# Kernel optimization log

Hardware: AMD Instinct MI355X
Metric: run time of the kernel (lower is better)

## Reference

```python
import jax, jax.numpy as jnp
import numpy as np


def setup_inputs() -> dict:
    key = jax.random.key(0)
    k1, k2, k3, k4 = jax.random.split(key, 4)
    B, T, E, H = 8, 2048, 1024, 64
    x = jax.random.normal(k1, (B, T, E), dtype=jnp.float32)
    # scale params like typical init to keep logits sane
    Wk = jax.random.normal(k2, (E, H), dtype=jnp.float32) * (E ** -0.5)
    Wq = jax.random.normal(k3, (E, H), dtype=jnp.float32) * (E ** -0.5)
    Wv = jax.random.normal(k4, (E, H), dtype=jnp.float32) * (E ** -0.5)
    return {"x": x, "Wk": Wk, "Wq": Wq, "Wv": Wv}


def reference(x, Wk, Wq, Wv):
    # x: [B, T, E]; Wk/Wq/Wv: [E, H]
    T = x.shape[1]
    H = Wk.shape[1]
    k = jnp.einsum('bte,eh->bth', x, Wk)
    q = jnp.einsum('bte,eh->bth', x, Wq)
    v = jnp.einsum('bte,eh->bth', x, Wv)
    # scaled scores [B, T, T]
    wei = jnp.einsum('bqh,bkh->bqk', q, k) * (H ** -0.5)
    causal = jnp.tril(jnp.ones((T, T), dtype=bool))  # tril buffer
    wei = jnp.where(causal, wei, -jnp.inf)
    wei = jax.nn.softmax(wei, axis=-1)
    # dropout p=0.0 (eval): identity
    return jnp.einsum('bqk,bkh->bqh', wei, v)
```

## Files before the change

kernel.cpp:

```cpp
#include <hip/hip_runtime.h>
#include <math.h>

constexpr int B_ = 8, T_ = 2048, E_ = 1024, H_ = 64;
constexpr long BT = (long)B_ * T_;

typedef __attribute__((ext_vector_type(8))) short bf16x8;
typedef __attribute__((ext_vector_type(4))) float f32x4;

__device__ inline unsigned short bf16_rne(float f) {
    union { float f; unsigned u; } v; v.f = f;
    unsigned u = v.u + (0x7FFFu + ((v.u >> 16) & 1u));
    return (unsigned short)(u >> 16);
}
__device__ inline unsigned pack_bf16x2(float lo, float hi) {
    unsigned r;
    asm("v_cvt_pk_bf16_f32 %0, %1, %2" : "=v"(r) : "v"(lo), "v"(hi));
    return r;
}

__device__ inline void load_lds16(const void* g, void* l) {
    __builtin_amdgcn_global_load_lds(
        (const __attribute__((address_space(1))) void*)(uintptr_t)g,
        (__attribute__((address_space(3))) void*)(unsigned)(uintptr_t)l,
        16, 0, 0);
}

constexpr float QS = 0.18033688011112042f;

__global__ __launch_bounds__(256) void wt_build_k(
    const float* __restrict__ Wk, const float* __restrict__ Wq,
    const float* __restrict__ Wv, unsigned short* __restrict__ Wt)
{
    const int d    = blockIdx.x * 256 + threadIdx.x;
    const int tile = d >> 6;
    const int lq   = d & 63;
    const int quad = lq >> 4;
    const int l16  = lq & 15;
    const int kc   = tile / 12;
    const int nt   = tile - kc * 12;
    const int n    = nt * 16 + l16;

    const float* src; int col; float s = 1.0f;
    if (n < 64)       { src = Wk; col = n; }
    else if (n < 128) { src = Wq; col = n - 64; s = QS; }
    else              { src = Wv; col = n - 128; }

    const int kk0 = kc * 32 + quad * 8;
    const float* sp = src + (size_t)kk0 * H_ + col;
    unsigned p[4];
    #pragma unroll
    for (int jj = 0; jj < 4; jj++)
        p[jj] = pack_bf16x2(sp[(2 * jj) * H_] * s, sp[(2 * jj + 1) * H_] * s);
    *(uint4*)(Wt + (size_t)d * 8) = make_uint4(p[0], p[1], p[2], p[3]);
}

struct Bfr { bf16x8 b0, b1, b2; };

__global__ __launch_bounds__(512) void qkv_mfma_k(
    const float* __restrict__ x, const unsigned short* __restrict__ Wt,
    unsigned short* __restrict__ kO, unsigned short* __restrict__ qO,
    unsigned short* __restrict__ vfO)
{
    __shared__ float4 xs[3][32][16];
    __shared__ unsigned short VL[32][66];

    const int t    = threadIdx.x;
    const int w    = t >> 6;
    const int l    = t & 63;
    const int l16  = l & 15;
    const int quad = l >> 4;
    const int rg   = w >> 2;
    const int nq   = w & 3;
    const int row0 = blockIdx.x * 32 + rg * 16;
    const int row0b = blockIdx.x * 32;

    const int rr = w * 4 + (l >> 4);
    const int cc = l & 15;
    const int gg = cc ^ (rr & 7);
    const float* gsrc = x + (size_t)(row0b + rr) * E_ + gg * 4;

    const int r  = rg * 16 + l16;
    const int rx = r & 7;

    auto LB = [&](int it, Bfr& F0, Bfr& F1) {
        const unsigned short* p0 = Wt + (size_t)((it * 2) * 12 + nq * 3) * 512 + (size_t)l * 8;
        F0.b0 = *(const bf16x8*)(p0);
        F0.b1 = *(const bf16x8*)(p0 + 512);
        F0.b2 = *(const bf16x8*)(p0 + 1024);
        const unsigned short* p1 = p0 + 12 * 512;
        F1.b0 = *(const bf16x8*)(p1);
        F1.b1 = *(const bf16x8*)(p1 + 512);
        F1.b2 = *(const bf16x8*)(p1 + 1024);
    };
    auto DMA = [&](int it) {
        load_lds16(gsrc + it * 64, &xs[it % 3][rr][cc]);
    };

    f32x4 acc[3];
    #pragma unroll
    for (int n = 0; n < 3; n++) acc[n] = (f32x4){0.f, 0.f, 0.f, 0.f};

    Bfr Bf[2][2];
    DMA(0);
    LB(0, Bf[0][0], Bf[0][1]);
    DMA(1);

    #pragma unroll
    for (int it = 0; it < 16; ++it) {
        if (it == 15) asm volatile("s_waitcnt vmcnt(6)" ::: "memory");
        else          asm volatile("s_waitcnt vmcnt(7)" ::: "memory");
        __builtin_amdgcn_s_barrier();
        __builtin_amdgcn_sched_barrier(0);

        if (it + 1 < 16) LB(it + 1, Bf[(it + 1) & 1][0], Bf[(it + 1) & 1][1]);
        if (it + 2 < 16) DMA(it + 2);

        const int pc = it & 1;
        const int bsel = it % 3;
        #pragma unroll
        for (int kk = 0; kk < 2; ++kk) {
            const int G0 = kk * 8 + quad * 2;
            float4 fa = xs[bsel][r][G0 ^ rx];
            float4 fb = xs[bsel][r][(G0 + 1) ^ rx];

            union { bf16x8 v; unsigned u[4]; } av;
            av.u[0] = pack_bf16x2(fa.x, fa.y);
            av.u[1] = pack_bf16x2(fa.z, fa.w);
            av.u[2] = pack_bf16x2(fb.x, fb.y);
            av.u[3] = pack_bf16x2(fb.z, fb.w);

            Bfr& F = Bf[pc][kk];
            acc[0] = __builtin_amdgcn_mfma_f32_16x16x32_bf16(av.v, F.b0, acc[0], 0, 0, 0);
            acc[1] = __builtin_amdgcn_mfma_f32_16x16x32_bf16(av.v, F.b1, acc[1], 0, 0, 0);
            acc[2] = __builtin_amdgcn_mfma_f32_16x16x32_bf16(av.v, F.b2, acc[2], 0, 0, 0);
        }
    }

    #pragma unroll
    for (int n = 0; n < 3; n++) {
        const int gn = nq * 3 + n;
        const int hb = gn * 16 + l16;
        if (gn < 4) {
            #pragma unroll
            for (int rr2 = 0; rr2 < 4; rr2++) {
                const int row = row0 + quad * 4 + rr2;
                kO[(size_t)row * H_ + hb] = bf16_rne(acc[n][rr2]);
            }
        } else if (gn < 8) {
            #pragma unroll
            for (int rr2 = 0; rr2 < 4; rr2++) {
                const int row = row0 + quad * 4 + rr2;
                qO[(size_t)row * H_ + (hb - 64)] = bf16_rne(acc[n][rr2]);
            }
        } else {
            #pragma unroll
            for (int rr2 = 0; rr2 < 4; rr2++)
                VL[rg * 16 + quad * 4 + rr2][(gn - 8) * 16 + l16] = bf16_rne(acc[n][rr2]);
        }
    }
    __syncthreads();

    if (t < 256) {
        const int g  = t >> 6;
        const int lf = t & 15;
        const int qf = (t >> 4) & 3;
        unsigned pk[4];
        #pragma unroll
        for (int jj = 0; jj < 4; jj++) {
            const int p0 = qf * 8 + 2 * jj;
            const int i0 = (p0 >> 1) | ((p0 & 1) << 4);
            const int p1 = p0 + 1;
            const int i1 = (p1 >> 1) | ((p1 & 1) << 4);
            pk[jj] = (unsigned)VL[i0][g * 16 + lf]
                   | ((unsigned)VL[i1][g * 16 + lf] << 16);
        }
        const int tile = blockIdx.x;
        *(uint4*)(vfO + ((size_t)tile * 4 + g) * 512 + (size_t)(t & 63) * 8) =
            make_uint4(pk[0], pk[1], pk[2], pk[3]);
    }
}

struct Kfr { bf16x8 k00, k01, k10, k11; };
struct Vfr { bf16x8 v0, v1, v2, v3; };

__global__ __launch_bounds__(512) void attn_mfma(
    const unsigned short* __restrict__ q,
    const unsigned short* __restrict__ k,
    const unsigned short* __restrict__ vf,
    float* __restrict__ out)
{
    __shared__ unsigned short Pl[8][2][16 * 40];
    __shared__ float Ot[8][16][68];
    __shared__ float LsW[8][16];

    const int t    = threadIdx.x;
    const int w    = t >> 6;
    const int l    = t & 63;
    const int l16  = l & 15;
    const int quad = l >> 4;

    const int b  = blockIdx.x & 7;
    const int p  = blockIdx.x >> 3;

    const unsigned short* kbp = k  + (size_t)b * T_ * H_ + (size_t)l16 * H_ + quad * 8;
    const unsigned short* vfb = vf + (size_t)b * 64 * 2048 + (size_t)l * 8;
    unsigned short* Pw0 = &Pl[w][0][0];
    unsigned short* Pw1 = &Pl[w][1][0];

    for (int ph = 0; ph < 2; ++ph) {
        const int qt = ph ? (127 - p) : p;
        const int t0 = qt * 16;
        const int nk = t0 / 32 + 1;

        const size_t qoff = ((size_t)b * T_ + t0 + l16) * H_ + quad * 8;
        bf16x8 aq0 = *(const bf16x8*)(q + qoff);
        bf16x8 aq1 = *(const bf16x8*)(q + qoff + 32);

        f32x4 o[4];
        #pragma unroll
        for (int g = 0; g < 4; g++) o[g] = (f32x4){0.f, 0.f, 0.f, 0.f};
        float ls[4] = {0.f, 0.f, 0.f, 0.f};

        auto LK = [&](int kt, Kfr& K) {
            const unsigned short* kp = kbp + (size_t)kt * 32 * H_;
            K.k00 = *(const bf16x8*)(kp);
            K.k01 = *(const bf16x8*)(kp + 32);
            K.k10 = *(const bf16x8*)(kp + 16 * H_);
            K.k11 = *(const bf16x8*)(kp + 16 * H_ + 32);
        };
        auto LV = [&](int kt, Vfr& V) {
            const unsigned short* vp = vfb + (size_t)kt * 2048;
            V.v0 = *(const bf16x8*)(vp);
            V.v1 = *(const bf16x8*)(vp + 512);
            V.v2 = *(const bf16x8*)(vp + 1024);
            V.v3 = *(const bf16x8*)(vp + 1536);
        };
        auto QKSM = [&](int kt, const Kfr& K, unsigned short* Pw) {
            f32x4 s0 = (f32x4){0.f, 0.f, 0.f, 0.f};
            f32x4 s1 = (f32x4){0.f, 0.f, 0.f, 0.f};
            s0 = __builtin_amdgcn_mfma_f32_16x16x32_bf16(aq0, K.k00, s0, 0, 0, 0);
            s0 = __builtin_amdgcn_mfma_f32_16x16x32_bf16(aq1, K.k01, s0, 0, 0, 0);
            s1 = __builtin_amdgcn_mfma_f32_16x16x32_bf16(aq0, K.k10, s1, 0, 0, 0);
            s1 = __builtin_amdgcn_mfma_f32_16x16x32_bf16(aq1, K.k11, s1, 0, 0, 0);
            const int kbase = kt * 32;
            if (kbase + 31 > t0) {
                const int rowb = t0 + quad * 4;
                #pragma unroll
                for (int r = 0; r < 4; r++) {
                    if (kbase + l16 > rowb + r)      s0[r] = -3.0e38f;
                    if (kbase + 16 + l16 > rowb + r) s1[r] = -3.0e38f;
                }
            }
            #pragma unroll
            for (int r = 0; r < 4; r++) {
                float p0 = exp2f(s0[r]);
                float p1 = exp2f(s1[r]);
                ls[r] += p0 + p1;
                *(unsigned*)(Pw + (quad * 4 + r) * 40 + 2 * l16) = pack_bf16x2(p0, p1);
            }
        };
        auto PRD = [&](const unsigned short* Pw) -> bf16x8 {
            return *(const bf16x8*)(Pw + l16 * 40 + quad * 8);
        };
        auto PV = [&](bf16x8 ap, const Vfr& V) {
            o[0] = __builtin_amdgcn_mfma_f32_16x16x32_bf16(ap, V.v0, o[0], 0, 0, 0);
            o[1] = __builtin_amdgcn_mfma_f32_16x16x32_bf16(ap, V.v1, o[1], 0, 0, 0);
            o[2] = __builtin_amdgcn_mfma_f32_16x16x32_bf16(ap, V.v2, o[2], 0, 0, 0);
            o[3] = __builtin_amdgcn_mfma_f32_16x16x32_bf16(ap, V.v3, o[3], 0, 0, 0);
        };

        int kt = w;
        if (kt < nk) {
            Kfr KA, KB; Vfr VA, VB;
            LK(kt, KA);
            if (kt + 8 < nk) LK(kt + 8, KB);
            LV(kt, VA);
            QKSM(kt, KA, Pw0);
            kt += 8;
            if (kt >= nk) {
                bf16x8 ap = PRD(Pw0);
                PV(ap, VA);
            } else {
                for (;;) {
                    if (kt + 8 < nk) LK(kt + 8, KA);
                    LV(kt, VB);
                    __builtin_amdgcn_sched_barrier(0);
                    { bf16x8 ap = PRD(Pw0); QKSM(kt, KB, Pw1); PV(ap, VA); }
                    kt += 8;
                    if (kt >= nk) { bf16x8 ap = PRD(Pw1); PV(ap, VB); break; }
                    if (kt + 8 < nk) LK(kt + 8, KB);
                    LV(kt, VA);
                    __builtin_amdgcn_sched_barrier(0);
                    { bf16x8 ap = PRD(Pw1); QKSM(kt, KA, Pw0); PV(ap, VB); }
                    kt += 8;
                    if (kt >= nk) { bf16x8 ap = PRD(Pw0); PV(ap, VA); break; }
                }
            }
        }

        #pragma unroll
        for (int r = 0; r < 4; r++) {
            float s = ls[r];
            s += __shfl_xor(s, 1);
            s += __shfl_xor(s, 2);
            s += __shfl_xor(s, 4);
            s += __shfl_xor(s, 8);
            ls[r] = s;
        }

        if (l16 == 0) {
            #pragma unroll
            for (int r = 0; r < 4; r++) LsW[w][quad * 4 + r] = ls[r];
        }
        #pragma unroll
        for (int g = 0; g < 4; g++)
            #pragma unroll
            for (int r = 0; r < 4; r++)
                Ot[w][quad * 4 + r][g * 16 + l16] = o[g][r];
        __syncthreads();

        {
            const int col = l;
            #pragma unroll
            for (int rr = 0; rr < 2; ++rr) {
                const int row = w * 2 + rr;
                float L = 0.f, sv = 0.f;
                #pragma unroll
                for (int w2 = 0; w2 < 8; ++w2) {
                    L  += LsW[w2][row];
                    sv += Ot[w2][row][col];
                }
                out[((size_t)b * T_ + t0 + row) * H_ + col] = sv / L;
            }
        }
        __syncthreads();
    }
}

extern "C" void kernel_launch(void* const* d_in, const int* in_sizes, int n_in,
                              void* d_out, int out_size, void* d_ws, size_t ws_size,
                              hipStream_t stream)
{
    const float* x  = (const float*)d_in[0];
    const float* Wk = (const float*)d_in[1];
    const float* Wq = (const float*)d_in[2];
    const float* Wv = (const float*)d_in[3];

    unsigned short* wt    = (unsigned short*)d_ws;
    unsigned short* kbuf  = wt + 24576 * 8;
    unsigned short* qbuf  = kbuf + BT * H_;
    unsigned short* vfbuf = qbuf + BT * H_;
    float* outp = (float*)d_out;

    wt_build_k<<<96, 256, 0, stream>>>(Wk, Wq, Wv, wt);
    qkv_mfma_k<<<(B_ * T_) / 32, 512, 0, stream>>>(x, wt, kbuf, qbuf, vfbuf);
    attn_mfma<<<512, 512, 0, stream>>>(qbuf, kbuf, vfbuf, outp);
}
```

Baseline: 140.4 us.

## Split attention over key chunks into partial blocks plus separate reduction kernel

Replaces the 512-block, 8-wave attention kernel, which paired light and heavy query tiles, with a split-K scheme. Each 256-thread block handles one 16-row query tile and one chunk of up to 8 key tiles, then writes unnormalized partial outputs and row sums to a workspace. A second kernel sums the chunks and normalizes. This aims to improve load balance and occupancy across CUs, at the cost of an extra launch, workspace traffic, many early-exiting empty blocks, and no software pipelining across key tiles within a wave.

```diff
diff --git a/kernel.cpp b/kernel.cpp
--- a/kernel.cpp
+++ b/kernel.cpp
@@ -183,15 +183,15 @@
 struct Kfr { bf16x8 k00, k01, k10, k11; };
 struct Vfr { bf16x8 v0, v1, v2, v3; };
 
-__global__ __launch_bounds__(512) void attn_mfma(
+__global__ __launch_bounds__(256) void attn_part(
     const unsigned short* __restrict__ q,
     const unsigned short* __restrict__ k,
     const unsigned short* __restrict__ vf,
-    float* __restrict__ out)
-{
-    __shared__ unsigned short Pl[8][2][16 * 40];
-    __shared__ float Ot[8][16][68];
-    __shared__ float LsW[8][16];
+    float* __restrict__ part)
+{
+    __shared__ unsigned short Pl[4][2][16 * 40];
+    __shared__ float Ot[4][16][68];
+    __shared__ float LsW[4][16];
 
     const int t    = threadIdx.x;
     const int w    = t >> 6;
@@ -200,141 +200,149 @@
     const int quad = l >> 4;
 
     const int b  = blockIdx.x & 7;
-    const int p  = blockIdx.x >> 3;
+    const int rblk = blockIdx.x >> 3;
+    const int qt = rblk / 9;
+    const int ci = rblk - qt * 9;
+
+    const int nk = qt / 2 + 1;
+    const int c  = (nk + 7) >> 3;
+    if (ci >= c) return;
+
+    const int t0  = qt * 16;
+    const int kt0 = ci * 8;
+    const int nt  = min(8, nk - kt0);
+
+    const size_t qoff = ((size_t)b * T_ + t0 + l16) * H_ + quad * 8;
+    bf16x8 aq0 = *(const bf16x8*)(q + qoff);
+    bf16x8 aq1 = *(const bf16x8*)(q + qoff + 32);
 
     const unsigned short* kbp = k  + (size_t)b * T_ * H_ + (size_t)l16 * H_ + quad * 8;
     const unsigned short* vfb = vf + (size_t)b * 64 * 2048 + (size_t)l * 8;
     unsigned short* Pw0 = &Pl[w][0][0];
     unsigned short* Pw1 = &Pl[w][1][0];
 
-    for (int ph = 0; ph < 2; ++ph) {
-        const int qt = ph ? (127 - p) : p;
-        const int t0 = qt * 16;
-        const int nk = t0 / 32 + 1;
-
-        const size_t qoff = ((size_t)b * T_ + t0 + l16) * H_ + quad * 8;
-        bf16x8 aq0 = *(const bf16x8*)(q + qoff);
-        bf16x8 aq1 = *(const bf16x8*)(q + qoff + 32);
-
-        f32x4 o[4];
-        #pragma unroll
-        for (int g = 0; g < 4; g++) o[g] = (f32x4){0.f, 0.f, 0.f, 0.f};
-        float ls[4] = {0.f, 0.f, 0.f, 0.f};
-
-        auto LK = [&](int kt, Kfr& K) {
-            const unsigned short* kp = kbp + (size_t)kt * 32 * H_;
-            K.k00 = *(const bf16x8*)(kp);
-            K.k01 = *(const bf16x8*)(kp + 32);
-            K.k10 = *(const bf16x8*)(kp + 16 * H_);
-            K.k11 = *(const bf16x8*)(kp + 16 * H_ + 32);
-        };
-        auto LV = [&](int kt, Vfr& V) {
-            const unsigned short* vp = vfb + (size_t)kt * 2048;
-            V.v0 = *(const bf16x8*)(vp);
-            V.v1 = *(const bf16x8*)(vp + 512);
-            V.v2 = *(const bf16x8*)(vp + 1024);
-            V.v3 = *(const bf16x8*)(vp + 1536);
-        };
-        auto QKSM = [&](int kt, const Kfr& K, unsigned short* Pw) {
-            f32x4 s0 = (f32x4){0.f, 0.f, 0.f, 0.f};
-            f32x4 s1 = (f32x4){0.f, 0.f, 0.f, 0.f};
-            s0 = __builtin_amdgcn_mfma_f32_16x16x32_bf16(aq0, K.k00, s0, 0, 0, 0);
-            s0 = __builtin_amdgcn_mfma_f32_16x16x32_bf16(aq1, K.k01, s0, 0, 0, 0);
-            s1 = __builtin_amdgcn_mfma_f32_16x16x32_bf16(aq0, K.k10, s1, 0, 0, 0);
-            s1 = __builtin_amdgcn_mfma_f32_16x16x32_bf16(aq1, K.k11, s1, 0, 0, 0);
-            const int kbase = kt * 32;
-            if (kbase + 31 > t0) {
-                const int rowb = t0 + quad * 4;
-                #pragma unroll
-                for (int r = 0; r < 4; r++) {
-                    if (kbase + l16 > rowb + r)      s0[r] = -3.0e38f;
-                    if (kbase + 16 + l16 > rowb + r) s1[r] = -3.0e38f;
-                }
-            }
+    f32x4 o[4];
+    #pragma unroll
+    for (int g = 0; g < 4; g++) o[g] = (f32x4){0.f, 0.f, 0.f, 0.f};
+    float ls[4] = {0.f, 0.f, 0.f, 0.f};
+
+    auto LK = [&](int kt, Kfr& K) {
+        const unsigned short* kp = kbp + (size_t)kt * 32 * H_;
+        K.k00 = *(const bf16x8*)(kp);
+        K.k01 = *(const bf16x8*)(kp + 32);
+        K.k10 = *(const bf16x8*)(kp + 16 * H_);
+        K.k11 = *(const bf16x8*)(kp + 16 * H_ + 32);
+    };
+    auto LV = [&](int kt, Vfr& V) {
+        const unsigned short* vp = vfb + (size_t)kt * 2048;
+        V.v0 = *(const bf16x8*)(vp);
+        V.v1 = *(const bf16x8*)(vp + 512);
+        V.v2 = *(const bf16x8*)(vp + 1024);
+        V.v3 = *(const bf16x8*)(vp + 1536);
+    };
+    auto QKSM = [&](int kt, const Kfr& K, unsigned short* Pw) {
+        f32x4 s0 = (f32x4){0.f, 0.f, 0.f, 0.f};
+        f32x4 s1 = (f32x4){0.f, 0.f, 0.f, 0.f};
+        s0 = __builtin_amdgcn_mfma_f32_16x16x32_bf16(aq0, K.k00, s0, 0, 0, 0);
+        s0 = __builtin_amdgcn_mfma_f32_16x16x32_bf16(aq1, K.k01, s0, 0, 0, 0);
+        s1 = __builtin_amdgcn_mfma_f32_16x16x32_bf16(aq0, K.k10, s1, 0, 0, 0);
+        s1 = __builtin_amdgcn_mfma_f32_16x16x32_bf16(aq1, K.k11, s1, 0, 0, 0);
+        const int kbase = kt * 32;
+        if (kbase + 31 > t0) {
+            const int rowb = t0 + quad * 4;
             #pragma unroll
             for (int r = 0; r < 4; r++) {
-                float p0 = exp2f(s0[r]);
-                float p1 = exp2f(s1[r]);
-                ls[r] += p0 + p1;
-                *(unsigned*)(Pw + (quad * 4 + r) * 40 + 2 * l16) = pack_bf16x2(p0, p1);
+                if (kbase + l16 > rowb + r)      s0[r] = -3.0e38f;
+                if (kbase + 16 + l16 > rowb + r) s1[r] = -3.0e38f;
             }
-        };
-        auto PRD = [&](const unsigned short* Pw) -> bf16x8 {
-            return *(const bf16x8*)(Pw + l16 * 40 + quad * 8);
-        };
-        auto PV = [&](bf16x8 ap, const Vfr& V) {
-            o[0] = __builtin_amdgcn_mfma_f32_16x16x32_bf16(ap, V.v0, o[0], 0, 0, 0);
-            o[1] = __builtin_amdgcn_mfma_f32_16x16x32_bf16(ap, V.v1, o[1], 0, 0, 0);
-            o[2] = __builtin_amdgcn_mfma_f32_16x16x32_bf16(ap, V.v2, o[2], 0, 0, 0);
-            o[3] = __builtin_amdgcn_mfma_f32_16x16x32_bf16(ap, V.v3, o[3], 0, 0, 0);
-        };
-
-        int kt = w;
-        if (kt < nk) {
-            Kfr KA, KB; Vfr VA, VB;
-            LK(kt, KA);
-            if (kt + 8 < nk) LK(kt + 8, KB);
-            LV(kt, VA);
-            QKSM(kt, KA, Pw0);
-            kt += 8;
-            if (kt >= nk) {
-                bf16x8 ap = PRD(Pw0);
-                PV(ap, VA);
-            } else {
-                for (;;) {
-                    if (kt + 8 < nk) LK(kt + 8, KA);
-                    LV(kt, VB);
-                    __builtin_amdgcn_sched_barrier(0);
-                    { bf16x8 ap = PRD(Pw0); QKSM(kt, KB, Pw1); PV(ap, VA); }
-                    kt += 8;
-                    if (kt >= nk) { bf16x8 ap = PRD(Pw1); PV(ap, VB); break; }
-                    if (kt + 8 < nk) LK(kt + 8, KB);
-                    LV(kt, VA);
-                    __builtin_amdgcn_sched_barrier(0);
-                    { bf16x8 ap = PRD(Pw1); QKSM(kt, KA, Pw0); PV(ap, VB); }
-                    kt += 8;
-                    if (kt >= nk) { bf16x8 ap = PRD(Pw0); PV(ap, VA); break; }
-                }
-            }
-        }
-
+        }
         #pragma unroll
         for (int r = 0; r < 4; r++) {
-            float s = ls[r];
-            s += __shfl_xor(s, 1);
-            s += __shfl_xor(s, 2);
-            s += __shfl_xor(s, 4);
-            s += __shfl_xor(s, 8);
-            ls[r] = s;
-        }
-
-        if (l16 == 0) {
-            #pragma unroll
-            for (int r = 0; r < 4; r++) LsW[w][quad * 4 + r] = ls[r];
-        }
-        #pragma unroll
-        for (int g = 0; g < 4; g++)
-            #pragma unroll
-            for (int r = 0; r < 4; r++)
-                Ot[w][quad * 4 + r][g * 16 + l16] = o[g][r];
-        __syncthreads();
-
-        {
-            const int col = l;
-            #pragma unroll
-            for (int rr = 0; rr < 2; ++rr) {
-                const int row = w * 2 + rr;
-                float L = 0.f, sv = 0.f;
-                #pragma unroll
-                for (int w2 = 0; w2 < 8; ++w2) {
-                    L  += LsW[w2][row];
-                    sv += Ot[w2][row][col];
-                }
-                out[((size_t)b * T_ + t0 + row) * H_ + col] = sv / L;
-            }
-        }
-        __syncthreads();
-    }
+            float p0 = exp2f(s0[r]);
+            float p1 = exp2f(s1[r]);
+            ls[r] += p0 + p1;
+            *(unsigned*)(Pw + (quad * 4 + r) * 40 + 2 * l16) = pack_bf16x2(p0, p1);
+        }
+    };
+    auto PV = [&](const unsigned short* Pw, const Vfr& V) {
+        asm volatile("s_waitcnt lgkmcnt(0)" ::: "memory");
+        bf16x8 ap = *(const bf16x8*)(Pw + l16 * 40 + quad * 8);
+        o[0] = __builtin_amdgcn_mfma_f32_16x16x32_bf16(ap, V.v0, o[0], 0, 0, 0);
+        o[1] = __builtin_amdgcn_mfma_f32_16x16x32_bf16(ap, V.v1, o[1], 0, 0, 0);
+        o[2] = __builtin_amdgcn_mfma_f32_16x16x32_bf16(ap, V.v2, o[2], 0, 0, 0);
+        o[3] = __builtin_amdgcn_mfma_f32_16x16x32_bf16(ap, V.v3, o[3], 0, 0, 0);
+    };
+
+    const int j0 = w, j1 = w + 4;
+    Kfr KA, KB; Vfr VA, VB;
+    if (j0 < nt) { LK(kt0 + j0, KA); LV(kt0 + j0, VA); }
+    if (j1 < nt) { LK(kt0 + j1, KB); LV(kt0 + j1, VB); }
+    __builtin_amdgcn_sched_barrier(0);
+    if (j0 < nt) { QKSM(kt0 + j0, KA, Pw0); PV(Pw0, VA); }
+    if (j1 < nt) { QKSM(kt0 + j1, KB, Pw1); PV(Pw1, VB); }
+
+    #pragma unroll
+    for (int r = 0; r < 4; r++) {
+        float s = ls[r];
+        s += __shfl_xor(s, 1);
+        s += __shfl_xor(s, 2);
+        s += __shfl_xor(s, 4);
+        s += __shfl_xor(s, 8);
+        ls[r] = s;
+    }
+
+    if (l16 == 0) {
+        #pragma unroll
+        for (int r = 0; r < 4; r++) LsW[w][quad * 4 + r] = ls[r];
+    }
+    #pragma unroll
+    for (int g = 0; g < 4; g++)
+        #pragma unroll
+        for (int r = 0; r < 4; r++)
+            Ot[w][quad * 4 + r][g * 16 + l16] = o[g][r];
+    __syncthreads();
+
+    float* slot = part + (size_t)blockIdx.x * 1040;
+    {
+        const int row = t >> 4;
+        const int c4  = (t & 15) * 4;
+        float4 sv = make_float4(0.f, 0.f, 0.f, 0.f);
+        #pragma unroll
+        for (int w2 = 0; w2 < 4; ++w2) {
+            sv.x += Ot[w2][row][c4 + 0];
+            sv.y += Ot[w2][row][c4 + 1];
+            sv.z += Ot[w2][row][c4 + 2];
+            sv.w += Ot[w2][row][c4 + 3];
+        }
+        *(float4*)(slot + row * 64 + c4) = sv;
+        if (t < 16)
+            slot[1024 + t] = LsW[0][t] + LsW[1][t] + LsW[2][t] + LsW[3][t];
+    }
+}
+
+__global__ __launch_bounds__(256) void attn_reduce(
+    const float* __restrict__ part, float* __restrict__ out)
+{
+    const int b  = blockIdx.x & 7;
+    const int qt = blockIdx.x >> 3;
+    const int nk = qt / 2 + 1;
+    const int c  = (nk + 7) >> 3;
+
+    const int t   = threadIdx.x;
+    const int row = t >> 4;
+    const int c4  = (t & 15) * 4;
+
+    float4 acc = make_float4(0.f, 0.f, 0.f, 0.f);
+    float L = 0.f;
+    for (int ci = 0; ci < c; ++ci) {
+        const float* slot = part + (size_t)(((qt * 9 + ci) << 3) + b) * 1040;
+        float4 v = *(const float4*)(slot + row * 64 + c4);
+        acc.x += v.x; acc.y += v.y; acc.z += v.z; acc.w += v.w;
+        L += slot[1024 + row];
+    }
+    const float inv = 1.0f / L;
+    float4 r = make_float4(acc.x * inv, acc.y * inv, acc.z * inv, acc.w * inv);
+    *(float4*)(out + ((size_t)b * T_ + qt * 16 + row) * H_ + c4) = r;
 }
 
 extern "C" void kernel_launch(void* const* d_in, const int* in_sizes, int n_in,
@@ -350,9 +358,11 @@
     unsigned short* kbuf  = wt + 24576 * 8;
     unsigned short* qbuf  = kbuf + BT * H_;
     unsigned short* vfbuf = qbuf + BT * H_;
+    float* part = (float*)(vfbuf + BT * H_);
     float* outp = (float*)d_out;
 
     wt_build_k<<<96, 256, 0, stream>>>(Wk, Wq, Wv, wt);
     qkv_mfma_k<<<(B_ * T_) / 32, 512, 0, stream>>>(x, wt, kbuf, qbuf, vfbuf);
-    attn_mfma<<<512, 512, 0, stream>>>(qbuf, kbuf, vfbuf, outp);
-}
+    attn_part<<<128 * 9 * 8, 256, 0, stream>>>(qbuf, kbuf, vfbuf, part);
+    attn_reduce<<<128 * 8, 256, 0, stream>>>(part, outp);
+}
```

Result: slower. 148.7 us (+6.0%).
